# Kernel optimization log

Measured on AMD Instinct MI355X. Metric: run time of the kernel, lower is better.

Reference implementation:

```python
import jax, jax.numpy as jnp
import numpy as np

DIM = 1024
DIM_HEAD = 64
HEADS = 16
BATCH = 2
SEQ = 2048
SCALE = DIM_HEAD ** -0.5


def setup_inputs() -> dict:
    key = jax.random.key(0)
    ks = jax.random.split(key, 5)
    tokens = jax.random.normal(ks[0], (BATCH, SEQ, DIM), dtype=jnp.float32)
    wq = jax.random.normal(ks[1], (HEADS, DIM, DIM_HEAD), dtype=jnp.float32)
    wk = jax.random.normal(ks[2], (HEADS, DIM, DIM_HEAD), dtype=jnp.float32)
    wv = jax.random.normal(ks[3], (HEADS, DIM, DIM_HEAD), dtype=jnp.float32)
    wo = jax.random.normal(ks[4], (HEADS, DIM_HEAD, DIM), dtype=jnp.float32)
    return {"tokens": tokens, "wq": wq, "wk": wk, "wv": wv, "wo": wo}


def reference(tokens, wq, wk, wv, wo):
    # q, k, v: [b, h, n, dh]
    q = jnp.einsum('bnd,hde->bhne', tokens, wq) * SCALE
    k = jnp.einsum('bnd,hde->bhne', tokens, wk)
    v = jnp.einsum('bnd,hde->bhne', tokens, wv)
    sim = jnp.einsum('bhie,bhje->bhij', q, k)          # [b, h, n, n]
    attn = jax.nn.softmax(sim, axis=-1)
    aggregated = jnp.einsum('bhij,bhje->bhie', attn, v)  # [b, h, n, dh]
    retrieved = jnp.einsum('bhne,hed->bnd', aggregated, wo)  # sum over heads
    return retrieved
```

## Files before the change

kernel.cpp:

```cpp
#include <hip/hip_runtime.h>
#include <hip/hip_fp16.h>
#include <stdint.h>

#define BB 2
#define HH 16
#define SS 2048
#define DD 1024
#define DHH 64
#define QSCALE 0.18033688011112042f

typedef _Float16 half8 __attribute__((ext_vector_type(8)));
typedef _Float16 half4 __attribute__((ext_vector_type(4)));
typedef __fp16 fp16x2 __attribute__((ext_vector_type(2)));
typedef float floatx4 __attribute__((ext_vector_type(4)));

__device__ __forceinline__ floatx4 mfma16(half8 a, half8 b, floatx4 c) {
  return __builtin_amdgcn_mfma_f32_16x16x32_f16(a, b, c, 0, 0, 0);
}
__device__ __forceinline__ floatx4 mfma16k16(half4 a, half4 b, floatx4 c) {
  return __builtin_amdgcn_mfma_f32_16x16x16f16(a, b, c, 0, 0, 0);
}

__device__ __forceinline__ void dma16(const _Float16* g, _Float16* l) {
  __builtin_amdgcn_global_load_lds(
      (const __attribute__((address_space(1))) uint32_t*)g,
      (__attribute__((address_space(3))) uint32_t*)l,
      16, 0, 0);
}

__global__ __launch_bounds__(256) void convert_kernel(
    const float* __restrict__ wq, const float* __restrict__ wk,
    const float* __restrict__ wv, const float* __restrict__ wo,
    _Float16* __restrict__ Wh, _Float16* __restrict__ Wl,
    _Float16* __restrict__ Wot)
{
  __shared__ float St[64][68];
  const int kt = blockIdx.x;
  const int hy = blockIdx.y;
  const int z  = blockIdx.z;
  const int t  = (int)threadIdx.x;
  const int k0 = kt * 64;

  const float* src = (z == 0) ? (wq + hy * (DD * DHH))
                   : (z == 1) ? (wk + hy * (DD * DHH))
                   : (z == 2) ? (wv + hy * (DD * DHH))
                   : wo;

  const int rr = t >> 4, cc = (t & 15) * 4;
  if (z < 3) {
    #pragma unroll
    for (int i = 0; i < 4; ++i)
      *(floatx4*)&St[rr + 16 * i][cc] =
          *(const floatx4*)(src + (k0 + rr + 16 * i) * DHH + cc);
  } else {
    const int d0 = hy * 64;
    #pragma unroll
    for (int i = 0; i < 4; ++i)
      *(floatx4*)&St[rr + 16 * i][cc] =
          *(const floatx4*)(src + (k0 + rr + 16 * i) * 1024 + d0 + cc);
  }
  __syncthreads();

  const int e = t >> 2, kc = (t & 3) * 16;
  if (z < 3) {
    const int n = z * 1024 + hy * 64 + e;
    half8 hi0, hi1, lo0, lo1;
    #pragma unroll
    for (int u = 0; u < 16; ++u) {
      float x = St[kc + u][e];
      _Float16 hh = (_Float16)x;
      _Float16 ll = (_Float16)(x - (float)hh);
      if (u < 8) { hi0[u] = hh; lo0[u] = ll; }
      else       { hi1[u - 8] = hh; lo1[u - 8] = ll; }
    }
    *(half8*)(Wh + n * 1024 + k0 + kc)     = hi0;
    *(half8*)(Wh + n * 1024 + k0 + kc + 8) = hi1;
    *(half8*)(Wl + n * 1024 + k0 + kc)     = lo0;
    *(half8*)(Wl + n * 1024 + k0 + kc + 8) = lo1;
  } else {
    const int d0 = hy * 64;
    half8 hi0, hi1;
    #pragma unroll
    for (int u = 0; u < 16; ++u) {
      _Float16 hh = (_Float16)St[kc + u][e];
      if (u < 8) hi0[u] = hh; else hi1[u - 8] = hh;
    }
    *(half8*)(Wot + (d0 + e) * 1024 + k0 + kc)     = hi0;
    *(half8*)(Wot + (d0 + e) * 1024 + k0 + kc + 8) = hi1;
  }
}

__global__ __launch_bounds__(256) void tokens_split_kernel(
    const float* __restrict__ tokens,
    _Float16* __restrict__ th, _Float16* __restrict__ tl)
{
  const int i = ((int)blockIdx.x * 256 + (int)threadIdx.x) * 8;
  floatx4 x0 = *(const floatx4*)(tokens + i);
  floatx4 x1 = *(const floatx4*)(tokens + i + 4);
  half8 h, l;
  #pragma unroll
  for (int j = 0; j < 8; ++j) {
    float x = (j < 4) ? x0[j] : x1[j - 4];
    _Float16 hh = (_Float16)x;
    h[j] = hh;
    l[j] = (_Float16)(x - (float)hh);
  }
  *(half8*)(th + i) = h;
  *(half8*)(tl + i) = l;
}

__global__ __launch_bounds__(256) void qkv_gemm_kernel(
    const _Float16* __restrict__ th, const _Float16* __restrict__ tl,
    const _Float16* __restrict__ Wh, const _Float16* __restrict__ Wl,
    _Float16* __restrict__ qh, _Float16* __restrict__ ql,
    _Float16* __restrict__ kh, _Float16* __restrict__ kl,
    _Float16* __restrict__ vt)
{
  __shared__ alignas(16) _Float16 sbuf[2][4][128 * 32];

  const int n0 = blockIdx.x * 128;
  const int m0 = blockIdx.y * 128;
  const int zb = n0 >> 10;
  const bool is_v = (zb == 2);
  const int t = (int)threadIdx.x;
  const int lane = t & 63, wid = t >> 6;
  const int l16 = lane & 15, q4 = lane >> 4;
  const int mw = (wid & 1) * 64, nw = (wid >> 1) * 64;

  const int g  = (lane & 7) ^ ((lane >> 3) & 7);
  const int grow  = (lane >> 3) * 2 + (g >> 2);
  const int gcol8 = (g & 3) * 8;
  const int laneoff = (l16 >> 1) * 128 + (((((l16 & 1) << 2) | q4) ^ (l16 >> 1)) * 16);

  const _Float16* src;
  int arr;
  if (wid == 0)      { src = th + m0 * 1024; arr = 0; }
  else if (wid == 1) { src = Wh + n0 * 1024; arr = 1; }
  else if (wid == 2) { src = Wl + n0 * 1024; arr = 2; }
  else               { src = tl + m0 * 1024; arr = 3; }
  const bool stage_active = !(is_v && wid == 3);
  const _Float16* gsrc = src + grow * 1024 + gcol8;

  const floatx4 z4 = {0.0f, 0.0f, 0.0f, 0.0f};
  floatx4 acc[4][4];
  #pragma unroll
  for (int mi = 0; mi < 4; ++mi)
    #pragma unroll
    for (int ni = 0; ni < 4; ++ni) acc[mi][ni] = z4;

  auto stage = [&](int buf, int kt2) {
    if (stage_active) {
      const _Float16* gp = gsrc + kt2 * 32;
      _Float16* dst = &sbuf[buf][arr][0];
      #pragma unroll
      for (int j = 0; j < 8; ++j)
        dma16(gp + j * 16 * 1024, dst + j * 16 * 32);
    }
  };

  auto compute = [&](int buf) {
    const char* sAh = (const char*)&sbuf[buf][0][0];
    const char* sBh = (const char*)&sbuf[buf][1][0];
    const char* sBl = (const char*)&sbuf[buf][2][0];
    const char* sAl = (const char*)&sbuf[buf][3][0];
    half8 a_h[4];
    #pragma unroll
    for (int mi = 0; mi < 4; ++mi)
      a_h[mi] = *(const half8*)(sAh + (mw + mi * 16) * 64 + laneoff);
    if (!is_v) {
      half8 a_l[4];
      #pragma unroll
      for (int mi = 0; mi < 4; ++mi)
        a_l[mi] = *(const half8*)(sAl + (mw + mi * 16) * 64 + laneoff);
      #pragma unroll
      for (int ni = 0; ni < 4; ++ni) {
        const half8 b_h = *(const half8*)(sBh + (nw + ni * 16) * 64 + laneoff);
        const half8 b_l = *(const half8*)(sBl + (nw + ni * 16) * 64 + laneoff);
        #pragma unroll
        for (int mi = 0; mi < 4; ++mi) {
          acc[mi][ni] = mfma16(a_h[mi], b_h, acc[mi][ni]);
          acc[mi][ni] = mfma16(a_h[mi], b_l, acc[mi][ni]);
          acc[mi][ni] = mfma16(a_l[mi], b_h, acc[mi][ni]);
        }
      }
    } else {
      #pragma unroll
      for (int ni = 0; ni < 4; ++ni) {
        const half8 b_h = *(const half8*)(sBh + (nw + ni * 16) * 64 + laneoff);
        const half8 b_l = *(const half8*)(sBl + (nw + ni * 16) * 64 + laneoff);
        #pragma unroll
        for (int mi = 0; mi < 4; ++mi) {
          acc[mi][ni] = mfma16(a_h[mi], b_h, acc[mi][ni]);
          acc[mi][ni] = mfma16(a_h[mi], b_l, acc[mi][ni]);
        }
      }
    }
  };

  stage(0, 0);
  __syncthreads();

  #pragma unroll 1
  for (int kt = 0; kt < 32; kt += 2) {
    if (kt + 1 < 32) stage(1, kt + 1);
    compute(0);
    __syncthreads();
    if (kt + 2 < 32) stage(0, kt + 2);
    compute(1);
    __syncthreads();
  }

  #pragma unroll
  for (int ni = 0; ni < 4; ++ni) {
    const int ncol = n0 + nw + ni * 16;
    const int h = (ncol >> 6) & 15;
    const int e = (ncol & 63) + l16;
    #pragma unroll
    for (int mi = 0; mi < 4; ++mi) {
      #pragma unroll
      for (int r = 0; r < 4; ++r) {
        const int grow2 = m0 + mw + mi * 16 + q4 * 4 + r;
        const int b = grow2 >> 11, s = grow2 & 2047;
        const float v = acc[mi][ni][r];
        const int qkidx = ((b * HH + h) * SS + s) * DHH + e;
        if (zb == 0) {
          const float vs = v * QSCALE;
          const _Float16 hh = (_Float16)vs;
          qh[qkidx] = hh;
          ql[qkidx] = (_Float16)(vs - (float)hh);
        } else if (zb == 1) {
          const _Float16 hh = (_Float16)v;
          kh[qkidx] = hh;
          kl[qkidx] = (_Float16)(v - (float)hh);
        } else {
          const int sl = s & 63;
          const int sp = (s & ~63) | ((sl & 48) >> 2) | ((sl & 12) << 2) | (sl & 3);
          vt[((b * HH + h) * DHH + e) * SS + sp] = (_Float16)v;
        }
      }
    }
  }
}

__global__ __launch_bounds__(512) void attn_kernel(
    const _Float16* __restrict__ qh, const _Float16* __restrict__ ql,
    const _Float16* __restrict__ kh, const _Float16* __restrict__ kl,
    const _Float16* __restrict__ vt, _Float16* __restrict__ agg)
{
  __shared__ _Float16 Kh[2][64][72], Kl[2][64][72];
  __shared__ _Float16 Vs[2][64][64];

  const int qt = blockIdx.x;
  const int h  = blockIdx.y;
  const int b  = blockIdx.z;
  const int bh = b * HH + h;
  const int t = (int)threadIdx.x;
  const int lane = t & 63, wid = t >> 6;
  const int l16 = lane & 15, q4 = lane >> 4;

  const int sr = t >> 3, sc = (t & 7) * 8;
  const int vsw = ((t & 7) ^ (sr & 7)) * 8;

  const int vch0 = ((2 * q4 + 0) ^ (l16 & 7)) * 8;
  const int vch1 = ((2 * q4 + 1) ^ (l16 & 7)) * 8;

  half8 qfh[2], qfl[2];
  {
    const int s = qt * 128 + wid * 16 + l16;
    const int base = (bh * SS + s) * DHH + q4 * 8;
    qfh[0] = *(const half8*)(qh + base);
    qfh[1] = *(const half8*)(qh + base + 32);
    qfl[0] = *(const half8*)(ql + base);
    qfl[1] = *(const half8*)(ql + base + 32);
  }

  const floatx4 z4 = {0.0f, 0.0f, 0.0f, 0.0f};
  floatx4 o[4];
  #pragma unroll
  for (int i = 0; i < 4; ++i) o[i] = z4;
  float m_r = -1e30f;
  float l_lane = 0.0f;

  half8 pK, pL, pV;
  {
    const int gk = (bh * SS + sr) * DHH + sc;
    pK = *(const half8*)(kh + gk);
    pL = *(const half8*)(kl + gk);
    pV = *(const half8*)(vt + (bh * DHH + sr) * SS + sc);
  }
  *(half8*)&Kh[0][sr][sc] = pK;
  *(half8*)&Kl[0][sr][sc] = pL;
  *(half8*)&Vs[0][sr][vsw] = pV;
  __syncthreads();
  {
    const int gk = (bh * SS + 64 + sr) * DHH + sc;
    pK = *(const half8*)(kh + gk);
    pL = *(const half8*)(kl + gk);
    pV = *(const half8*)(vt + (bh * DHH + sr) * SS + 64 + sc);
  }

  auto body = [&](int buf, int kt) {
    floatx4 sv[4];
    __builtin_amdgcn_s_setprio(1);
    #pragma unroll
    for (int sub = 0; sub < 4; ++sub) {
      const half8 ah0 = *(const half8*)&Kh[buf][sub * 16 + l16][q4 * 8];
      const half8 ah1 = *(const half8*)&Kh[buf][sub * 16 + l16][q4 * 8 + 32];
      const half8 al0 = *(const half8*)&Kl[buf][sub * 16 + l16][q4 * 8];
      const half8 al1 = *(const half8*)&Kl[buf][sub * 16 + l16][q4 * 8 + 32];
      floatx4 s4 = z4;
      s4 = mfma16(ah0, qfh[0], s4);
      s4 = mfma16(ah1, qfh[1], s4);
      s4 = mfma16(al0, qfh[0], s4);
      s4 = mfma16(al1, qfh[1], s4);
      s4 = mfma16(ah0, qfl[0], s4);
      s4 = mfma16(ah1, qfl[1], s4);
      sv[sub] = s4;
    }
    __builtin_amdgcn_s_setprio(0);

    float m0 = fmaxf(fmaxf(sv[0][0], sv[0][1]), fmaxf(sv[0][2], sv[0][3]));
    float m1 = fmaxf(fmaxf(sv[1][0], sv[1][1]), fmaxf(sv[1][2], sv[1][3]));
    float m2 = fmaxf(fmaxf(sv[2][0], sv[2][1]), fmaxf(sv[2][2], sv[2][3]));
    float m3 = fmaxf(fmaxf(sv[3][0], sv[3][1]), fmaxf(sv[3][2], sv[3][3]));
    const float mx = fmaxf(fmaxf(m0, m1), fmaxf(m2, m3));

    if (__any(mx > m_r + 8.0f)) {
      float mc = fmaxf(mx, __shfl_xor(mx, 16));
      mc = fmaxf(mc, __shfl_xor(mc, 32));
      const float mnew = fmaxf(m_r, mc);
      const float alpha = exp2f(m_r - mnew);
      m_r = mnew;
      l_lane *= alpha;
      #pragma unroll
      for (int sub = 0; sub < 4; ++sub)
        #pragma unroll
        for (int r = 0; r < 4; ++r) o[sub][r] *= alpha;
    }

    half4 p4[4];
    #pragma unroll
    for (int c = 0; c < 4; ++c) {
      const float p0 = exp2f(sv[c][0] - m_r);
      const float p1 = exp2f(sv[c][1] - m_r);
      const float p2 = exp2f(sv[c][2] - m_r);
      const float p3 = exp2f(sv[c][3] - m_r);
      l_lane += (p0 + p1) + (p2 + p3);
      const fp16x2 a01 = __builtin_amdgcn_cvt_pkrtz(p0, p1);
      const fp16x2 a23 = __builtin_amdgcn_cvt_pkrtz(p2, p3);
      half4 pv;
      pv[0] = (_Float16)a01[0]; pv[1] = (_Float16)a01[1];
      pv[2] = (_Float16)a23[0]; pv[3] = (_Float16)a23[1];
      p4[c] = pv;
    }

    if (kt < 31) {
      *(half8*)&Kh[buf ^ 1][sr][sc] = pK;
      *(half8*)&Kl[buf ^ 1][sr][sc] = pL;
      *(half8*)&Vs[buf ^ 1][sr][vsw] = pV;
    }

    __builtin_amdgcn_s_setprio(1);
    #pragma unroll
    for (int sub = 0; sub < 4; ++sub) {
      const half8 v01 = *(const half8*)&Vs[buf][sub * 16 + l16][vch0];
      const half8 v23 = *(const half8*)&Vs[buf][sub * 16 + l16][vch1];
      const half4 va0 = {v01[0], v01[1], v01[2], v01[3]};
      const half4 va1 = {v01[4], v01[5], v01[6], v01[7]};
      const half4 va2 = {v23[0], v23[1], v23[2], v23[3]};
      const half4 va3 = {v23[4], v23[5], v23[6], v23[7]};
      o[sub] = mfma16k16(va0, p4[0], o[sub]);
      o[sub] = mfma16k16(va1, p4[1], o[sub]);
      o[sub] = mfma16k16(va2, p4[2], o[sub]);
      o[sub] = mfma16k16(va3, p4[3], o[sub]);
    }
    __builtin_amdgcn_s_setprio(0);

    __syncthreads();

    if (kt < 30) {
      const int k2 = (kt + 2) * 64;
      const int gk = (bh * SS + k2 + sr) * DHH + sc;
      pK = *(const half8*)(kh + gk);
      pL = *(const half8*)(kl + gk);
      pV = *(const half8*)(vt + (bh * DHH + sr) * SS + k2 + sc);
    }
  };

  #pragma unroll 1
  for (int kt = 0; kt < 32; kt += 2) {
    body(0, kt);
    body(1, kt + 1);
  }

  float lsum = l_lane;
  lsum += __shfl_xor(lsum, 16);
  lsum += __shfl_xor(lsum, 32);
  const float inv = 1.0f / lsum;
  const int s = qt * 128 + wid * 16 + l16;
  #pragma unroll
  for (int sub = 0; sub < 4; ++sub) {
    half4 ov;
    #pragma unroll
    for (int r = 0; r < 4; ++r) ov[r] = (_Float16)(o[sub][r] * inv);
    *(half4*)(agg + (b * SS + s) * (HH * DHH) + h * DHH + sub * 16 + q4 * 4) = ov;
  }
}

__global__ __launch_bounds__(256) void out_gemm_kernel(
    const _Float16* __restrict__ agg, const _Float16* __restrict__ Wot,
    float* __restrict__ out)
{
  __shared__ alignas(16) _Float16 sbuf[2][2][128 * 32];
  const int n0 = blockIdx.x * 128;
  const int m0 = blockIdx.y * 128;
  const int t = (int)threadIdx.x;
  const int lane = t & 63, wid = t >> 6;
  const int l16 = lane & 15, q4 = lane >> 4;
  const int mw = (wid & 1) * 64, nw = (wid >> 1) * 64;

  const int g  = (lane & 7) ^ ((lane >> 3) & 7);
  const int grow  = (lane >> 3) * 2 + (g >> 2);
  const int gcol8 = (g & 3) * 8;
  const int laneoff = (l16 >> 1) * 128 + (((((l16 & 1) << 2) | q4) ^ (l16 >> 1)) * 16);

  const int arr = wid >> 1;
  const int half64 = (wid & 1) * 64;
  const _Float16* src = (arr == 0) ? (agg + m0 * 1024) : (Wot + n0 * 1024);
  const _Float16* gsrc = src + (half64 + grow) * 1024 + gcol8;

  const floatx4 z4 = {0.0f, 0.0f, 0.0f, 0.0f};
  floatx4 acc[4][4];
  #pragma unroll
  for (int mi = 0; mi < 4; ++mi)
    #pragma unroll
    for (int ni = 0; ni < 4; ++ni) acc[mi][ni] = z4;

  auto stage = [&](int buf, int kt2) {
    const _Float16* gp = gsrc + kt2 * 32;
    _Float16* dst = &sbuf[buf][arr][half64 * 32];
    #pragma unroll
    for (int j = 0; j < 4; ++j)
      dma16(gp + j * 16 * 1024, dst + j * 16 * 32);
  };

  auto compute = [&](int buf) {
    const char* sA = (const char*)&sbuf[buf][0][0];
    const char* sB = (const char*)&sbuf[buf][1][0];
    half8 a_f[4];
    #pragma unroll
    for (int mi = 0; mi < 4; ++mi)
      a_f[mi] = *(const half8*)(sA + (mw + mi * 16) * 64 + laneoff);
    #pragma unroll
    for (int ni = 0; ni < 4; ++ni) {
      const half8 b_f = *(const half8*)(sB + (nw + ni * 16) * 64 + laneoff);
      #pragma unroll
      for (int mi = 0; mi < 4; ++mi)
        acc[mi][ni] = mfma16(a_f[mi], b_f, acc[mi][ni]);
    }
  };

  stage(0, 0);
  __syncthreads();

  #pragma unroll 1
  for (int kt = 0; kt < 32; kt += 2) {
    if (kt + 1 < 32) stage(1, kt + 1);
    compute(0);
    __syncthreads();
    if (kt + 2 < 32) stage(0, kt + 2);
    compute(1);
    __syncthreads();
  }

  #pragma unroll
  for (int ni = 0; ni < 4; ++ni)
    #pragma unroll
    for (int mi = 0; mi < 4; ++mi)
      #pragma unroll
      for (int r = 0; r < 4; ++r)
        out[(m0 + mw + mi * 16 + q4 * 4 + r) * 1024 + n0 + nw + ni * 16 + l16] =
            acc[mi][ni][r];
}

extern "C" void kernel_launch(void* const* d_in, const int* in_sizes, int n_in,
                              void* d_out, int out_size, void* d_ws, size_t ws_size,
                              hipStream_t stream)
{
  const float* tokens = (const float*)d_in[0];
  const float* wq = (const float*)d_in[1];
  const float* wk = (const float*)d_in[2];
  const float* wv = (const float*)d_in[3];
  const float* wo = (const float*)d_in[4];
  float* out = (float*)d_out;

  char* ws = (char*)d_ws;
  _Float16* qh  = (_Float16*)(ws);
  _Float16* ql  = (_Float16*)(ws + 8388608);
  _Float16* kh  = (_Float16*)(ws + 16777216);
  _Float16* kl  = (_Float16*)(ws + 25165824);
  _Float16* vt  = (_Float16*)(ws + 33554432);
  _Float16* Wh  = (_Float16*)(ws + 41943040);
  _Float16* Wl  = (_Float16*)(ws + 48234496);
  _Float16* Wot = (_Float16*)(ws + 54525952);
  _Float16* th  = (_Float16*)(ws + 56623104);
  _Float16* tl  = (_Float16*)(ws + 65011712);
  _Float16* agg = (_Float16*)(ws + 56623104);

  convert_kernel<<<dim3(16, 16, 4), 256, 0, stream>>>(wq, wk, wv, wo, Wh, Wl, Wot);
  tokens_split_kernel<<<2048, 256, 0, stream>>>(tokens, th, tl);
  qkv_gemm_kernel<<<dim3(24, 32), 256, 0, stream>>>(th, tl, Wh, Wl, qh, ql, kh, kl, vt);
  attn_kernel<<<dim3(16, 16, 2), 512, 0, stream>>>(qh, ql, kh, kl, vt, agg);
  out_gemm_kernel<<<dim3(8, 32), 256, 0, stream>>>(agg, Wot, out);
}
```

Before: 279.0 us.

## Halve QKV GEMM LDS by reading low-part operands from global; shrink out-GEMM M tile

In the QKV GEMM, only the high fp16 halves of tokens and weights are staged through LDS. The low-order correction operands (tl, Wl) are now read straight from global memory into registers inside the compute step. This halves shared memory per block, and launch bounds request 4 blocks per CU to raise occupancy, at the cost of uncoalesced-ish global fragment loads inside the inner loop. Separately, the output GEMM uses a 64-row M tile with double the grid, so more blocks can spread across the CUs, but only 3 of 4 waves do staging and each block gets less reuse.

```diff
diff --git a/kernel.cpp b/kernel.cpp
--- a/kernel.cpp
+++ b/kernel.cpp
@@ -109,14 +109,14 @@
   *(half8*)(tl + i) = l;
 }
 
-__global__ __launch_bounds__(256) void qkv_gemm_kernel(
+__global__ __launch_bounds__(256, 4) void qkv_gemm_kernel(
     const _Float16* __restrict__ th, const _Float16* __restrict__ tl,
     const _Float16* __restrict__ Wh, const _Float16* __restrict__ Wl,
     _Float16* __restrict__ qh, _Float16* __restrict__ ql,
     _Float16* __restrict__ kh, _Float16* __restrict__ kl,
     _Float16* __restrict__ vt)
 {
-  __shared__ alignas(16) _Float16 sbuf[2][4][128 * 32];
+  __shared__ alignas(16) _Float16 sbuf[2][2][128 * 32];
 
   const int n0 = blockIdx.x * 128;
   const int m0 = blockIdx.y * 128;
@@ -132,14 +132,13 @@
   const int gcol8 = (g & 3) * 8;
   const int laneoff = (l16 >> 1) * 128 + (((((l16 & 1) << 2) | q4) ^ (l16 >> 1)) * 16);
 
-  const _Float16* src;
-  int arr;
-  if (wid == 0)      { src = th + m0 * 1024; arr = 0; }
-  else if (wid == 1) { src = Wh + n0 * 1024; arr = 1; }
-  else if (wid == 2) { src = Wl + n0 * 1024; arr = 2; }
-  else               { src = tl + m0 * 1024; arr = 3; }
-  const bool stage_active = !(is_v && wid == 3);
-  const _Float16* gsrc = src + grow * 1024 + gcol8;
+  const int arr = wid >> 1;
+  const int rh  = (wid & 1) * 64;
+  const _Float16* src = (arr == 0) ? (th + m0 * 1024) : (Wh + n0 * 1024);
+  const _Float16* gsrc = src + (rh + grow) * 1024 + gcol8;
+
+  const _Float16* alrow = tl + (m0 + mw + l16) * 1024 + q4 * 8;
+  const _Float16* blrow = Wl + (n0 + nw + l16) * 1024 + q4 * 8;
 
   const floatx4 z4 = {0.0f, 0.0f, 0.0f, 0.0f};
   floatx4 acc[4][4];
@@ -149,51 +148,45 @@
     for (int ni = 0; ni < 4; ++ni) acc[mi][ni] = z4;
 
   auto stage = [&](int buf, int kt2) {
-    if (stage_active) {
-      const _Float16* gp = gsrc + kt2 * 32;
-      _Float16* dst = &sbuf[buf][arr][0];
-      #pragma unroll
-      for (int j = 0; j < 8; ++j)
-        dma16(gp + j * 16 * 1024, dst + j * 16 * 32);
-    }
+    const _Float16* gp = gsrc + kt2 * 32;
+    _Float16* dst = &sbuf[buf][arr][rh * 32];
+    #pragma unroll
+    for (int j = 0; j < 4; ++j)
+      dma16(gp + j * 16 * 1024, dst + j * 16 * 32);
   };
 
-  auto compute = [&](int buf) {
+  auto compute = [&](int buf, int kt) {
     const char* sAh = (const char*)&sbuf[buf][0][0];
     const char* sBh = (const char*)&sbuf[buf][1][0];
-    const char* sBl = (const char*)&sbuf[buf][2][0];
-    const char* sAl = (const char*)&sbuf[buf][3][0];
-    half8 a_h[4];
+    half8 a_h[4], b_h[4];
     #pragma unroll
     for (int mi = 0; mi < 4; ++mi)
       a_h[mi] = *(const half8*)(sAh + (mw + mi * 16) * 64 + laneoff);
+    #pragma unroll
+    for (int ni = 0; ni < 4; ++ni)
+      b_h[ni] = *(const half8*)(sBh + (nw + ni * 16) * 64 + laneoff);
+
+    #pragma unroll
+    for (int ni = 0; ni < 4; ++ni)
+      #pragma unroll
+      for (int mi = 0; mi < 4; ++mi)
+        acc[mi][ni] = mfma16(a_h[mi], b_h[ni], acc[mi][ni]);
+
     if (!is_v) {
-      half8 a_l[4];
+      #pragma unroll
+      for (int mi = 0; mi < 4; ++mi) {
+        const half8 al = *(const half8*)(alrow + mi * 16 * 1024 + kt * 32);
+        #pragma unroll
+        for (int ni = 0; ni < 4; ++ni)
+          acc[mi][ni] = mfma16(al, b_h[ni], acc[mi][ni]);
+      }
+    }
+    #pragma unroll
+    for (int ni = 0; ni < 4; ++ni) {
+      const half8 bl = *(const half8*)(blrow + ni * 16 * 1024 + kt * 32);
       #pragma unroll
       for (int mi = 0; mi < 4; ++mi)
-        a_l[mi] = *(const half8*)(sAl + (mw + mi * 16) * 64 + laneoff);
-      #pragma unroll
-      for (int ni = 0; ni < 4; ++ni) {
-        const half8 b_h = *(const half8*)(sBh + (nw + ni * 16) * 64 + laneoff);
-        const half8 b_l = *(const half8*)(sBl + (nw + ni * 16) * 64 + laneoff);
-        #pragma unroll
-        for (int mi = 0; mi < 4; ++mi) {
-          acc[mi][ni] = mfma16(a_h[mi], b_h, acc[mi][ni]);
-          acc[mi][ni] = mfma16(a_h[mi], b_l, acc[mi][ni]);
-          acc[mi][ni] = mfma16(a_l[mi], b_h, acc[mi][ni]);
-        }
-      }
-    } else {
-      #pragma unroll
-      for (int ni = 0; ni < 4; ++ni) {
-        const half8 b_h = *(const half8*)(sBh + (nw + ni * 16) * 64 + laneoff);
-        const half8 b_l = *(const half8*)(sBl + (nw + ni * 16) * 64 + laneoff);
-        #pragma unroll
-        for (int mi = 0; mi < 4; ++mi) {
-          acc[mi][ni] = mfma16(a_h[mi], b_h, acc[mi][ni]);
-          acc[mi][ni] = mfma16(a_h[mi], b_l, acc[mi][ni]);
-        }
-      }
+        acc[mi][ni] = mfma16(a_h[mi], bl, acc[mi][ni]);
     }
   };
 
@@ -203,10 +196,10 @@
   #pragma unroll 1
   for (int kt = 0; kt < 32; kt += 2) {
     if (kt + 1 < 32) stage(1, kt + 1);
-    compute(0);
+    compute(0, kt);
     __syncthreads();
     if (kt + 2 < 32) stage(0, kt + 2);
-    compute(1);
+    compute(1, kt + 1);
     __syncthreads();
   }
 
@@ -411,51 +404,54 @@
     const _Float16* __restrict__ agg, const _Float16* __restrict__ Wot,
     float* __restrict__ out)
 {
-  __shared__ alignas(16) _Float16 sbuf[2][2][128 * 32];
+  __shared__ alignas(16) _Float16 sA[2][64 * 32];
+  __shared__ alignas(16) _Float16 sB[2][128 * 32];
   const int n0 = blockIdx.x * 128;
-  const int m0 = blockIdx.y * 128;
+  const int m0 = blockIdx.y * 64;
   const int t = (int)threadIdx.x;
   const int lane = t & 63, wid = t >> 6;
   const int l16 = lane & 15, q4 = lane >> 4;
-  const int mw = (wid & 1) * 64, nw = (wid >> 1) * 64;
+  const int mw = (wid & 1) * 32, nw = (wid >> 1) * 64;
 
   const int g  = (lane & 7) ^ ((lane >> 3) & 7);
   const int grow  = (lane >> 3) * 2 + (g >> 2);
   const int gcol8 = (g & 3) * 8;
   const int laneoff = (l16 >> 1) * 128 + (((((l16 & 1) << 2) | q4) ^ (l16 >> 1)) * 16);
 
-  const int arr = wid >> 1;
-  const int half64 = (wid & 1) * 64;
-  const _Float16* src = (arr == 0) ? (agg + m0 * 1024) : (Wot + n0 * 1024);
-  const _Float16* gsrc = src + (half64 + grow) * 1024 + gcol8;
+  const bool stage_active = (wid < 3);
+  const int rh = (wid == 2) ? 64 : 0;
+  const _Float16* src = (wid == 0) ? (agg + m0 * 1024) : (Wot + n0 * 1024);
+  const _Float16* gsrc = src + (rh + grow) * 1024 + gcol8;
 
   const floatx4 z4 = {0.0f, 0.0f, 0.0f, 0.0f};
-  floatx4 acc[4][4];
-  #pragma unroll
-  for (int mi = 0; mi < 4; ++mi)
+  floatx4 acc[2][4];
+  #pragma unroll
+  for (int mi = 0; mi < 2; ++mi)
     #pragma unroll
     for (int ni = 0; ni < 4; ++ni) acc[mi][ni] = z4;
 
   auto stage = [&](int buf, int kt2) {
-    const _Float16* gp = gsrc + kt2 * 32;
-    _Float16* dst = &sbuf[buf][arr][half64 * 32];
-    #pragma unroll
-    for (int j = 0; j < 4; ++j)
-      dma16(gp + j * 16 * 1024, dst + j * 16 * 32);
+    if (stage_active) {
+      const _Float16* gp = gsrc + kt2 * 32;
+      _Float16* dst = (wid == 0) ? &sA[buf][0] : &sB[buf][rh * 32];
+      #pragma unroll
+      for (int j = 0; j < 4; ++j)
+        dma16(gp + j * 16 * 1024, dst + j * 16 * 32);
+    }
   };
 
   auto compute = [&](int buf) {
-    const char* sA = (const char*)&sbuf[buf][0][0];
-    const char* sB = (const char*)&sbuf[buf][1][0];
-    half8 a_f[4];
-    #pragma unroll
-    for (int mi = 0; mi < 4; ++mi)
-      a_f[mi] = *(const half8*)(sA + (mw + mi * 16) * 64 + laneoff);
+    const char* sAp = (const char*)&sA[buf][0];
+    const char* sBp = (const char*)&sB[buf][0];
+    half8 a_f[2];
+    #pragma unroll
+    for (int mi = 0; mi < 2; ++mi)
+      a_f[mi] = *(const half8*)(sAp + (mw + mi * 16) * 64 + laneoff);
     #pragma unroll
     for (int ni = 0; ni < 4; ++ni) {
-      const half8 b_f = *(const half8*)(sB + (nw + ni * 16) * 64 + laneoff);
-      #pragma unroll
-      for (int mi = 0; mi < 4; ++mi)
+      const half8 b_f = *(const half8*)(sBp + (nw + ni * 16) * 64 + laneoff);
+      #pragma unroll
+      for (int mi = 0; mi < 2; ++mi)
         acc[mi][ni] = mfma16(a_f[mi], b_f, acc[mi][ni]);
     }
   };
@@ -476,7 +472,7 @@
   #pragma unroll
   for (int ni = 0; ni < 4; ++ni)
     #pragma unroll
-    for (int mi = 0; mi < 4; ++mi)
+    for (int mi = 0; mi < 2; ++mi)
       #pragma unroll
       for (int r = 0; r < 4; ++r)
         out[(m0 + mw + mi * 16 + q4 * 4 + r) * 1024 + n0 + nw + ni * 16 + l16] =
@@ -511,5 +507,5 @@
   tokens_split_kernel<<<2048, 256, 0, stream>>>(tokens, th, tl);
   qkv_gemm_kernel<<<dim3(24, 32), 256, 0, stream>>>(th, tl, Wh, Wl, qh, ql, kh, kl, vt);
   attn_kernel<<<dim3(16, 16, 2), 512, 0, stream>>>(qh, ql, kh, kl, vt, agg);
-  out_gemm_kernel<<<dim3(8, 32), 256, 0, stream>>>(agg, Wot, out);
-}
+  out_gemm_kernel<<<dim3(8, 64), 256, 0, stream>>>(agg, Wot, out);
+}
```

New measurement: 332.8 us. 1.19x slower.

## Deepen QKV GEMM pipeline to four LDS stages with vmcnt-based waits

Applied to the files above, without the earlier changes.

Replaces the double-buffered QKV GEMM main loop with a four-buffer ring that prefetches three k-tiles ahead. It waits on outstanding DMA loads with s_waitcnt vmcnt and issues a single barrier per k-step instead of __syncthreads. The compute body is also reordered to load all B fragments up front and issue the MFMAs in grouped passes (hi*hi, lo*hi, hi*lo), sharing more code between the V and Q/K paths. LDS use doubles to 128 KB per block, which may reduce occupancy, in exchange for hiding more global-load latency.

```diff
diff --git a/kernel.cpp b/kernel.cpp
--- a/kernel.cpp
+++ b/kernel.cpp
@@ -116,7 +116,7 @@
     _Float16* __restrict__ kh, _Float16* __restrict__ kl,
     _Float16* __restrict__ vt)
 {
-  __shared__ alignas(16) _Float16 sbuf[2][4][128 * 32];
+  __shared__ alignas(16) _Float16 sbuf[4][4][128 * 32];
 
   const int n0 = blockIdx.x * 128;
   const int m0 = blockIdx.y * 128;
@@ -163,52 +163,60 @@
     const char* sBh = (const char*)&sbuf[buf][1][0];
     const char* sBl = (const char*)&sbuf[buf][2][0];
     const char* sAl = (const char*)&sbuf[buf][3][0];
-    half8 a_h[4];
+    half8 a_h[4], b_h[4], b_l[4];
     #pragma unroll
     for (int mi = 0; mi < 4; ++mi)
       a_h[mi] = *(const half8*)(sAh + (mw + mi * 16) * 64 + laneoff);
+    #pragma unroll
+    for (int ni = 0; ni < 4; ++ni) {
+      b_h[ni] = *(const half8*)(sBh + (nw + ni * 16) * 64 + laneoff);
+      b_l[ni] = *(const half8*)(sBl + (nw + ni * 16) * 64 + laneoff);
+    }
+    #pragma unroll
+    for (int ni = 0; ni < 4; ++ni)
+      #pragma unroll
+      for (int mi = 0; mi < 4; ++mi)
+        acc[mi][ni] = mfma16(a_h[mi], b_h[ni], acc[mi][ni]);
     if (!is_v) {
       half8 a_l[4];
       #pragma unroll
       for (int mi = 0; mi < 4; ++mi)
         a_l[mi] = *(const half8*)(sAl + (mw + mi * 16) * 64 + laneoff);
       #pragma unroll
-      for (int ni = 0; ni < 4; ++ni) {
-        const half8 b_h = *(const half8*)(sBh + (nw + ni * 16) * 64 + laneoff);
-        const half8 b_l = *(const half8*)(sBl + (nw + ni * 16) * 64 + laneoff);
+      for (int ni = 0; ni < 4; ++ni)
         #pragma unroll
-        for (int mi = 0; mi < 4; ++mi) {
-          acc[mi][ni] = mfma16(a_h[mi], b_h, acc[mi][ni]);
-          acc[mi][ni] = mfma16(a_h[mi], b_l, acc[mi][ni]);
-          acc[mi][ni] = mfma16(a_l[mi], b_h, acc[mi][ni]);
-        }
-      }
-    } else {
-      #pragma unroll
-      for (int ni = 0; ni < 4; ++ni) {
-        const half8 b_h = *(const half8*)(sBh + (nw + ni * 16) * 64 + laneoff);
-        const half8 b_l = *(const half8*)(sBl + (nw + ni * 16) * 64 + laneoff);
-        #pragma unroll
-        for (int mi = 0; mi < 4; ++mi) {
-          acc[mi][ni] = mfma16(a_h[mi], b_h, acc[mi][ni]);
-          acc[mi][ni] = mfma16(a_h[mi], b_l, acc[mi][ni]);
-        }
-      }
-    }
+        for (int mi = 0; mi < 4; ++mi)
+          acc[mi][ni] = mfma16(a_l[mi], b_h[ni], acc[mi][ni]);
+    }
+    #pragma unroll
+    for (int ni = 0; ni < 4; ++ni)
+      #pragma unroll
+      for (int mi = 0; mi < 4; ++mi)
+        acc[mi][ni] = mfma16(a_h[mi], b_l[ni], acc[mi][ni]);
   };
 
   stage(0, 0);
-  __syncthreads();
+  stage(1, 1);
+  stage(2, 2);
+
+#define QKV_PHASE(P, BUF, VC)                                  \
+  asm volatile("s_waitcnt vmcnt(" #VC ")" ::: "memory");       \
+  __builtin_amdgcn_s_barrier();                                \
+  if ((P) + 3 < 32) stage(((P) + 3) & 3, (P) + 3);             \
+  compute(BUF);
 
   #pragma unroll 1
-  for (int kt = 0; kt < 32; kt += 2) {
-    if (kt + 1 < 32) stage(1, kt + 1);
-    compute(0);
-    __syncthreads();
-    if (kt + 2 < 32) stage(0, kt + 2);
-    compute(1);
-    __syncthreads();
-  }
+  for (int p4 = 0; p4 < 28; p4 += 4) {
+    QKV_PHASE(p4 + 0, 0, 16)
+    QKV_PHASE(p4 + 1, 1, 16)
+    QKV_PHASE(p4 + 2, 2, 16)
+    QKV_PHASE(p4 + 3, 3, 16)
+  }
+  QKV_PHASE(28, 0, 16)
+  QKV_PHASE(29, 1, 16)
+  QKV_PHASE(30, 2, 8)
+  QKV_PHASE(31, 3, 0)
+#undef QKV_PHASE
 
   #pragma unroll
   for (int ni = 0; ni < 4; ++ni) {
```

New measurement: 285.4 us. +2.3%, slower.
